# Kernel optimization log

Measured on AMD Instinct MI355X. Metric: run time of the kernel, lower is better.

The kernel has to match this reference:

```python
import jax, jax.numpy as jnp
import numpy as np

F = 256       # num_features
H = 128       # hidden_dim
B = 2048      # batch
K = 15        # max_ratios
EPS = 1e-8


def setup_inputs() -> dict:
    key = jax.random.key(0)
    ks = jax.random.split(key, 13)
    def lin(k, fan_in, fan_out):
        bound = 1.0 / np.sqrt(fan_in)
        return jax.random.uniform(k, (fan_in, fan_out), jnp.float32, -bound, bound)
    inp = {
        "x": jax.random.normal(ks[0], (B, F), jnp.float32),
        # ratio_selector: F -> H -> F*F (sigmoid)
        "rs_w1": lin(ks[1], F, H), "rs_b1": jnp.zeros((H,), jnp.float32),
        "rs_w2": lin(ks[2], H, F * F), "rs_b2": jnp.zeros((F * F,), jnp.float32),
        # operation_selector: F -> H -> 4 (softmax)
        "os_w1": lin(ks[3], F, H), "os_b1": jnp.zeros((H,), jnp.float32),
        "os_w2": lin(ks[4], H, 4), "os_b2": jnp.zeros((4,), jnp.float32),
        # feature_transform: F -> H -> F
        "ft_w1": lin(ks[5], F, H), "ft_b1": jnp.zeros((H,), jnp.float32),
        "ft_w2": lin(ks[6], H, F), "ft_b2": jnp.zeros((F,), jnp.float32),
    }
    return inp


def reference(x, rs_w1, rs_b1, rs_w2, rs_b2, os_w1, os_b1, os_w2, os_b2,
              ft_w1, ft_b1, ft_w2, ft_b2):
    nf = x.shape[1]

    # feature_transform (dropout=0 -> identity)
    tf = jax.nn.relu(x @ ft_w1 + ft_b1) @ ft_w2 + ft_b2          # [B, F]
    # ratio_selector -> sigmoid selection weights over F*F pairs
    sel = jax.nn.sigmoid(jax.nn.relu(x @ rs_w1 + rs_b1) @ rs_w2 + rs_b2)  # [B, F*F]
    # operation_selector -> softmax over 4 ops
    op_w = jax.nn.softmax(jax.nn.relu(x @ os_w1 + os_b1) @ os_w2 + os_b2, axis=-1)  # [B, 4]

    top_k = min(K, sel.shape[1])
    top_values, top_indices = jax.lax.top_k(sel, top_k)          # [B, K]

    i_idx = top_indices // nf                                    # [B, K]
    j_idx = top_indices % nf
    fi = jnp.take_along_axis(tf, i_idx, axis=1)                  # [B, K]
    fj = jnp.take_along_axis(tf, j_idx, axis=1)

    ratio = fi / (jnp.abs(fj) + EPS)
    log_ratio = jnp.log(jnp.abs(fi) + EPS) - jnp.log(jnp.abs(fj) + EPS)
    diff = fi - fj
    prod = fi * fj
    ops = jnp.stack([ratio, log_ratio, diff, prod], axis=-1)     # [B, K, 4]
    ratio_tensor = jnp.sum(ops * op_w[:, None, :], axis=-1)      # [B, K]

    pair_importances = jnp.mean(top_values, axis=0)              # [K]
    op_prefs = jnp.mean(op_w, axis=0)                            # [4]
    ratio_mags = jnp.mean(jnp.abs(ratio_tensor), axis=0)         # [K]
    sel_entropy = jnp.mean(-jnp.sum(sel * jnp.log(sel + 1e-8), axis=1))

    return ratio_tensor, pair_importances, op_prefs, ratio_mags, sel_entropy
```

## Files before the change

kernel.cpp:

```cpp
#include <hip/hip_runtime.h>
#include <math.h>

#define BB 2048
#define FD 256
#define HD 128
#define FF 65536
#define TK 15
#define BCAP 1024
#define MAXCH 4
#define POISON (1 << 30)
#define NEG_INF (-3.4e38f)
#define EPSF 1e-8f
#define ZCLAMP 1.4f

typedef short short8 __attribute__((ext_vector_type(8)));
typedef float f32x4  __attribute__((ext_vector_type(4)));

__device__ __forceinline__ unsigned short bf16_rne(float x) {
  unsigned u = __float_as_uint(x);
  unsigned r = u + 0x7FFFu + ((u >> 16) & 1u);
  return (unsigned short)(r >> 16);
}

#define HC0 3.4657359e-01f
#define HC1 (-7.6713203e-02f)
#define HC2 (-6.25e-02f)
#define HC3 1.6809444e-02f
#define HC4 7.8125e-03f
#define HC5 (-2.4621900e-03f)
#define HC6 (-8.6805556e-04f)
#define HC7 3.0960500e-04f
#define HC8 9.2231000e-05f

__device__ __forceinline__ float hpoly(float zc) {
  float p = HC8;
  p = fmaf(p, zc, HC7); p = fmaf(p, zc, HC6); p = fmaf(p, zc, HC5);
  p = fmaf(p, zc, HC4); p = fmaf(p, zc, HC3); p = fmaf(p, zc, HC2);
  p = fmaf(p, zc, HC1); p = fmaf(p, zc, HC0);
  return p;
}

__global__ __launch_bounds__(256) void k1_front(
    const float* __restrict__ x,
    const float* __restrict__ rs_w1, const float* __restrict__ rs_b1,
    const float* __restrict__ rs_w2, const float* __restrict__ rs_b2,
    const float* __restrict__ os_w1, const float* __restrict__ os_b1,
    const float* __restrict__ os_w2, const float* __restrict__ os_b2,
    const float* __restrict__ ft_w1, const float* __restrict__ ft_b1,
    const float* __restrict__ ft_w2, const float* __restrict__ ft_b2,
    float* __restrict__ hrs, unsigned short* __restrict__ hb,
    float* __restrict__ tf, float* __restrict__ opw,
    float* __restrict__ tau, int* __restrict__ gcnt)
{
  __shared__ float xs[4 * FD];
  __shared__ float hft[4][HD];
  __shared__ float hos[4][HD];
  __shared__ float hl[4 * HD];
  __shared__ float lg[4][4];
  __shared__ float wred[4][4][2];
  const int tid = threadIdx.x;
  const int wave = tid >> 6, lane = tid & 63;
  const int r0  = blockIdx.x * 4;

  if (tid < 4) gcnt[blockIdx.x * 4 + tid] = 0;

  for (int i = tid; i < 4 * FD; i += 256) xs[i] = x[(size_t)r0 * FD + i];
  __syncthreads();

  {
    const int h    = tid & (HD - 1);
    const int half = tid >> 7;
    const int ra = 2 * half, rb = ra + 1;
    float a0=0.f,a1=0.f,b0=0.f,b1=0.f,c0=0.f,c1=0.f;
    for (int f = 0; f < FD; ++f) {
      const float wr = rs_w1[f*HD+h], wf = ft_w1[f*HD+h], wo = os_w1[f*HD+h];
      const float x0 = xs[ra*FD+f],   x1 = xs[rb*FD+f];
      a0 = fmaf(x0,wr,a0); a1 = fmaf(x1,wr,a1);
      b0 = fmaf(x0,wf,b0); b1 = fmaf(x1,wf,b1);
      c0 = fmaf(x0,wo,c0); c1 = fmaf(x1,wo,c1);
    }
    const float brs = rs_b1[h], bft = ft_b1[h], bos = os_b1[h];
    const float va = fmaxf(a0 + brs, 0.f), vb = fmaxf(a1 + brs, 0.f);
    hrs[(size_t)(r0+ra)*HD + h] = va;
    hrs[(size_t)(r0+rb)*HD + h] = vb;
    hb[(size_t)(r0+ra)*HD + h] = bf16_rne(va);
    hb[(size_t)(r0+rb)*HD + h] = bf16_rne(vb);
    hl[ra*HD + h] = va;
    hl[rb*HD + h] = vb;
    hft[ra][h] = fmaxf(b0 + bft, 0.f);
    hft[rb][h] = fmaxf(b1 + bft, 0.f);
    hos[ra][h] = fmaxf(c0 + bos, 0.f);
    hos[rb][h] = fmaxf(c1 + bos, 0.f);
  }
  __syncthreads();

  {
    const int c = tid;
    const float bb = ft_b2[c];
    float t0=bb,t1=bb,t2=bb,t3=bb;
    for (int h = 0; h < HD; ++h) {
      const float w = ft_w2[h*FD + c];
      t0 = fmaf(hft[0][h],w,t0); t1 = fmaf(hft[1][h],w,t1);
      t2 = fmaf(hft[2][h],w,t2); t3 = fmaf(hft[3][h],w,t3);
    }
    tf[(size_t)(r0+0)*FD+c]=t0; tf[(size_t)(r0+1)*FD+c]=t1;
    tf[(size_t)(r0+2)*FD+c]=t2; tf[(size_t)(r0+3)*FD+c]=t3;
  }

  if (tid < 16) {
    const int r = tid >> 2, o = tid & 3;
    float a = os_b2[o];
    for (int h = 0; h < HD; ++h) a = fmaf(hos[r][h], os_w2[h*4 + o], a);
    lg[r][o] = a;
  }
  __syncthreads();
  if (tid < 16) {
    const int r = tid >> 2, o = tid & 3;
    const float m = fmaxf(fmaxf(lg[r][0],lg[r][1]), fmaxf(lg[r][2],lg[r][3]));
    const float e = __expf(lg[r][o]-m);
    const float s = __expf(lg[r][0]-m)+__expf(lg[r][1]-m)+__expf(lg[r][2]-m)+__expf(lg[r][3]-m);
    opw[(size_t)(r0+r)*4+o] = e/s;
  }

  {
    const int c0 = tid * 4;
    float z[4][4];
    const float4 bb = *(const float4*)(rs_b2 + c0);
#pragma unroll
    for (int r = 0; r < 4; ++r) { z[r][0]=bb.x; z[r][1]=bb.y; z[r][2]=bb.z; z[r][3]=bb.w; }
    for (int k = 0; k < HD; ++k) {
      const float4 ww = *(const float4*)(rs_w2 + (size_t)k * FF + c0);
#pragma unroll
      for (int r = 0; r < 4; ++r) {
        const float a = hl[r * HD + k];
        z[r][0] = fmaf(a, ww.x, z[r][0]);
        z[r][1] = fmaf(a, ww.y, z[r][1]);
        z[r][2] = fmaf(a, ww.z, z[r][2]);
        z[r][3] = fmaf(a, ww.w, z[r][3]);
      }
    }
#pragma unroll
    for (int r = 0; r < 4; ++r) {
      float s1 = z[r][0] + z[r][1] + z[r][2] + z[r][3];
      float s2 = z[r][0]*z[r][0] + z[r][1]*z[r][1] + z[r][2]*z[r][2] + z[r][3]*z[r][3];
#pragma unroll
      for (int d = 1; d < 64; d <<= 1) { s1 += __shfl_xor(s1, d); s2 += __shfl_xor(s2, d); }
      if (lane == 0) { wred[wave][r][0] = s1; wred[wave][r][1] = s2; }
    }
    __syncthreads();
    if (tid < 4) {
      const float s1 = wred[0][tid][0]+wred[1][tid][0]+wred[2][tid][0]+wred[3][tid][0];
      const float s2 = wred[0][tid][1]+wred[1][tid][1]+wred[2][tid][1]+wred[3][tid][1];
      const float mu  = s1 * (1.f / 1024.f);
      const float var = fmaxf(s2 * (1.f / 1024.f) - mu * mu, 0.f);
      const float sd  = sqrtf(var);
      tau[r0 + tid] = (sd > 1e-6f * (fabsf(mu) + 1e-6f)) ? (mu + 3.1f * sd) : NEG_INF;
    }
  }
}

__global__ __launch_bounds__(256, 3) void k2_sel(
    const float* __restrict__ W2, const float* __restrict__ b2,
    const float* __restrict__ hrs, const unsigned short* __restrict__ hb,
    const float* __restrict__ tau,
    int* __restrict__ gcnt, float* __restrict__ gz, int* __restrict__ gi,
    float* __restrict__ ent_part, int capr)
{
  __shared__ uint4 Blds[2][16][64];
  __shared__ int   cands[BCAP];
  __shared__ float tau_l[512];
  __shared__ int   bcnt;
  __shared__ float entred[4];

  const int tid  = threadIdx.x;
  const int wave = tid >> 6, lane = tid & 63;
  const int n16  = lane & 15, quad = lane >> 4;
  const int xcd = blockIdx.x & 7, jj = blockIdx.x >> 3;
  const int cc  = ((jj >> 2) << 3) | xcd, rs = jj & 3;
  const int c0  = cc * 128, rbase = rs * 512;
  const int half = wave & 1, wrow0 = (wave >> 1) * 64;
  const int wcol0 = half * 64;

  if (tid == 0) bcnt = 0;
  tau_l[tid] = tau[rbase + tid];
  tau_l[tid + 256] = tau[rbase + 256 + tid];

  for (int p = 0; p < 8; ++p) {
    const int pid = p * 256 + tid;
    const int bh = pid >> 10;
    const int rest = pid & 1023;
    const int bct = rest >> 8, bks = (rest >> 6) & 3, bln = rest & 63;
    const int bn16 = bln & 15, bqd = bln >> 4;
    const int col = c0 + bh * 64 + bct * 16 + bn16;
    const int k0 = bks * 32 + bqd * 8;
    short8 f;
#pragma unroll
    for (int u = 0; u < 8; ++u)
      f[u] = (short)bf16_rne(W2[(size_t)(k0 + u) * FF + col]);
    Blds[bh][bct * 4 + bks][bln] = __builtin_bit_cast(uint4, f);
  }
  __syncthreads();

  float bv[4];
#pragma unroll
  for (int ct = 0; ct < 4; ++ct) bv[ct] = b2[c0 + wcol0 + ct * 16 + n16];

  float ent = 0.f;

  for (int mt = 0; mt < 4; ++mt) {
#pragma unroll
    for (int rh = 0; rh < 2; ++rh) {
      const int hrow = rbase + mt * 128 + wrow0 + rh * 32;

      f32x4 acc[2][4];
#pragma unroll
      for (int rt = 0; rt < 2; ++rt)
#pragma unroll
        for (int ct = 0; ct < 4; ++ct) acc[rt][ct] = (f32x4){0.f, 0.f, 0.f, 0.f};

#pragma unroll
      for (int ks = 0; ks < 4; ++ks) {
        short8 af[2], bfr[4];
#pragma unroll
        for (int rt = 0; rt < 2; ++rt)
          af[rt] = __builtin_bit_cast(short8,
              *(const uint4*)(hb + (size_t)(hrow + rt * 16 + n16) * HD + ks * 32 + quad * 8));
#pragma unroll
        for (int ct = 0; ct < 4; ++ct)
          bfr[ct] = __builtin_bit_cast(short8, Blds[half][ct * 4 + ks][lane]);
#pragma unroll
        for (int rt = 0; rt < 2; ++rt)
#pragma unroll
          for (int ct = 0; ct < 4; ++ct)
            acc[rt][ct] = __builtin_amdgcn_mfma_f32_16x16x32_bf16(
                af[rt], bfr[ct], acc[rt][ct], 0, 0, 0);
      }

      float zmax = 0.f;
#pragma unroll
      for (int rt = 0; rt < 2; ++rt) {
        const int rl0 = mt * 128 + wrow0 + rh * 32 + rt * 16 + quad * 4;
        const f32x4 tl = *(const f32x4*)&tau_l[rl0];
#pragma unroll
        for (int ct = 0; ct < 4; ++ct) {
#pragma unroll
          for (int rg = 0; rg < 4; ++rg) {
            const float z = acc[rt][ct][rg] + bv[ct];
            zmax = fmaxf(zmax, __builtin_fabsf(z));
            const float zc = fminf(fmaxf(z, -ZCLAMP), ZCLAMP);
            ent -= hpoly(zc);
            if (__any(z >= tl[rg])) {
              if (z >= tl[rg]) {
                const int q  = atomicAdd(&bcnt, 1);
                const int gm = rl0 + rg;
                if (q < BCAP) cands[q] = (gm << 7) | (wcol0 + ct * 16 + n16);
                else atomicOr(&gcnt[rbase + gm], POISON);
              }
            }
          }
        }
      }
      if (__any(zmax > ZCLAMP)) {
#pragma unroll
        for (int rt = 0; rt < 2; ++rt)
#pragma unroll
          for (int ct = 0; ct < 4; ++ct)
#pragma unroll
            for (int rg = 0; rg < 4; ++rg) {
              const float z = acc[rt][ct][rg] + bv[ct];
              if (__builtin_fabsf(z) > ZCLAMP) {
                const float zc = fminf(fmaxf(z, -ZCLAMP), ZCLAMP);
                const float zx = fmaxf(z, -60.f);
                const float w = 1.f + __expf(-zx);
                ent += hpoly(zc) - __logf(w) * __builtin_amdgcn_rcpf(w);
              }
            }
      }
    }
  }

  __syncthreads();
  {
    const int nc = min(bcnt, BCAP);
    const int grp = tid >> 4, gl = tid & 15;
    for (int ci = grp; ci < nc; ci += 16) {
      const int pk = cands[ci];
      const int r = rbase + (pk >> 7), c = c0 + (pk & 127);
      float s = 0.f;
      const int k0 = gl * 8;
#pragma unroll
      for (int u = 0; u < 8; ++u)
        s = fmaf(hrs[(size_t)r * HD + k0 + u], W2[(size_t)(k0 + u) * FF + c], s);
#pragma unroll
      for (int d = 1; d < 16; d <<= 1) s += __shfl_xor(s, d);
      if (gl == 0) {
        const float z = s + b2[c];
        const int pos = atomicAdd(&gcnt[r], 1);
        if (pos < capr) {
          gz[(size_t)r * capr + pos] = z;
          gi[(size_t)r * capr + pos] = c;
        }
      }
    }
  }

#pragma unroll
  for (int off = 32; off >= 1; off >>= 1) ent += __shfl_down(ent, off);
  if (lane == 0) entred[wave] = ent;
  __syncthreads();
  if (tid == 0) ent_part[blockIdx.x] = entred[0] + entred[1] + entred[2] + entred[3];
}

__global__ __launch_bounds__(256) void k3_select(
    const int* __restrict__ gcnt, const float* __restrict__ gz, const int* __restrict__ gi,
    const float* __restrict__ tau,
    const float* __restrict__ hrs, const float* __restrict__ W2, const float* __restrict__ b2,
    const float* __restrict__ tf, const float* __restrict__ opw,
    float* __restrict__ out_rt, float* __restrict__ pi_part, float* __restrict__ mag_part,
    int capr)
{
  __shared__ float csv[4][MAXCH][16];
  __shared__ int   csi[4][MAXCH][16];
  __shared__ float tv[4][TK];
  __shared__ int   ti[4][TK];
  __shared__ float s_pi[4][TK];
  __shared__ float s_mag[4][TK];
  __shared__ float red_v[256];
  __shared__ int   red_i[256];
  __shared__ float hrow[HD];
  __shared__ int   fb_w[4];
  __shared__ int   fb_n;

  const int tid  = threadIdx.x;
  const int wave = tid >> 6, lane = tid & 63;
  const int row  = blockIdx.x * 4 + wave;
  if (tid == 0) fb_n = 0;
  __syncthreads();

  const int raw = gcnt[row];
  const float tau_r = tau[row];
  int okflag = (raw >= TK && raw <= capr) ? 1 : 0;

  if (okflag) {
    const int nch = (raw + 63) >> 6;
    for (int ch = 0; ch < nch; ++ch) {
      const int sl = ch * 64 + lane;
      float v; int ix;
      if (sl < raw) {
        const float z = gz[(size_t)row * capr + sl];
        v  = 1.f / (1.f + __expf(-z));
        ix = gi[(size_t)row * capr + sl];
      } else { v = -1.f; ix = 0x7fffffff; }
#pragma unroll
      for (int k = 2; k <= 64; k <<= 1) {
#pragma unroll
        for (int j = k >> 1; j >= 1; j >>= 1) {
          const float pv = __shfl_xor(v, j);
          const int   pj = __shfl_xor(ix, j);
          const bool up    = ((lane & k) == 0);
          const bool lower = ((lane & j) == 0);
          const bool gt = (v > pv) || (v == pv && ix < pj);
          const bool keep = (lower == up) ? gt : !gt;
          if (!keep) { v = pv; ix = pj; }
        }
      }
      if (lane < 16) { csv[wave][ch][lane] = v; csi[wave][ch][lane] = ix; }
    }
    if (lane == 0) {
      int p[MAXCH];
#pragma unroll
      for (int i = 0; i < MAXCH; ++i) p[i] = 0;
      for (int round = 0; round < TK; ++round) {
        float bvv = -2.f; int bi = 0x7fffffff; int bw = 0;
        for (int ch = 0; ch < nch; ++ch) {
          if (p[ch] < 16) {
            const float vv = csv[wave][ch][p[ch]];
            const int   ii = csi[wave][ch][p[ch]];
            if (vv > bvv || (vv == bvv && ii < bi)) { bvv = vv; bi = ii; bw = ch; }
          }
        }
        ++p[bw];
        tv[wave][round] = bvv; ti[wave][round] = bi;
      }
      const float stau = 1.f / (1.f + __expf(-tau_r));
      if (tv[wave][TK - 1] < stau) okflag = 0;
    }
    okflag = __shfl(okflag, 0);
  }
  if (!okflag && lane == 0) { const int q = atomicAdd(&fb_n, 1); fb_w[q] = wave; }
  __syncthreads();

  const int nfb = fb_n;
  for (int f = 0; f < nfb; ++f) {
    const int w = fb_w[f];
    const int frow = blockIdx.x * 4 + w;
    for (int i = tid; i < HD; i += 256) hrow[i] = hrs[(size_t)frow * HD + i];
    __syncthreads();
    float kv[TK]; int ki[TK];
#pragma unroll
    for (int q = 0; q < TK; ++q) { kv[q] = -2.f; ki[q] = 0x7fffffff; }
    for (int u = 0; u < FF / 256; ++u) {
      const int c = u * 256 + tid;
      float z = b2[c];
      for (int k = 0; k < HD; ++k) z = fmaf(hrow[k], W2[(size_t)k * FF + c], z);
      const float s = 1.f / (1.f + __expf(-z));
      if (s > kv[TK-1] || (s == kv[TK-1] && c < ki[TK-1])) {
        float cv = s; int cc2 = c;
#pragma unroll
        for (int q = 0; q < TK; ++q) {
          const bool bet = (cv > kv[q]) || (cv == kv[q] && cc2 < ki[q]);
          const float tq = kv[q]; const int tj = ki[q];
          if (bet) { kv[q] = cv; ki[q] = cc2; cv = tq; cc2 = tj; }
        }
      }
    }
    int pi = 0;
    for (int round = 0; round < TK; ++round) {
      red_v[tid] = (pi < TK) ? kv[pi] : -2.f;
      red_i[tid] = (pi < TK) ? ki[pi] : 0x7fffffff;
      __syncthreads();
      for (int off = 128; off >= 1; off >>= 1) {
        if (tid < off) {
          const float ov = red_v[tid + off]; const int oi = red_i[tid + off];
          if (ov > red_v[tid] || (ov == red_v[tid] && oi < red_i[tid])) {
            red_v[tid] = ov; red_i[tid] = oi;
          }
        }
        __syncthreads();
      }
      const float wv = red_v[0]; const int wi = red_i[0];
      __syncthreads();
      if (pi < TK && ki[pi] == wi) ++pi;
      if (tid == 0) { tv[w][round] = wv; ti[w][round] = wi; }
    }
    __syncthreads();
  }
  __syncthreads();

  if (lane < TK) {
    const float rv = tv[wave][lane];
    const int j = ti[wave][lane], ii = j >> 8, jj = j & 255;
    const float fi = tf[(size_t)row * FD + ii];
    const float fj = tf[(size_t)row * FD + jj];
    const float* w = opw + (size_t)row * 4;
    const float ratio = fi / (fabsf(fj) + EPSF);
    const float lr    = logf(fabsf(fi) + EPSF) - logf(fabsf(fj) + EPSF);
    const float rt    = ratio * w[0] + lr * w[1] + (fi - fj) * w[2] + fi * fj * w[3];
    out_rt[(size_t)row * TK + lane] = rt;
    s_pi[wave][lane]  = rv;
    s_mag[wave][lane] = fabsf(rt);
  }
  __syncthreads();
  if (tid < TK) {
    pi_part[(size_t)blockIdx.x * TK + tid]  = s_pi[0][tid]+s_pi[1][tid]+s_pi[2][tid]+s_pi[3][tid];
    mag_part[(size_t)blockIdx.x * TK + tid] = s_mag[0][tid]+s_mag[1][tid]+s_mag[2][tid]+s_mag[3][tid];
  }
}

__global__ __launch_bounds__(256) void k4_final(
    const float* __restrict__ pi_part, const float* __restrict__ mag_part,
    const float* __restrict__ opw, const float* __restrict__ ent_part,
    float* __restrict__ out)
{
  __shared__ float red[256];
  const int tid = threadIdx.x;
  const int NB3 = BB / 4;
  const int base = BB * TK;
  const int sec = blockIdx.x;

  if (sec == 0) {
    const int r = tid & 15, seg = tid >> 4;
    float s = 0.f;
    if (r < TK) for (int q = seg; q < NB3; q += 16) s += pi_part[(size_t)q * TK + r];
    red[tid] = s; __syncthreads();
    if (tid < TK) { float t = 0.f; for (int g = 0; g < 16; ++g) t += red[g*16 + tid];
      out[base + tid] = t / (float)BB; }
  } else if (sec == 1) {
    const int r = tid & 15, seg = tid >> 4;
    float s = 0.f;
    if (r < TK) for (int q = seg; q < NB3; q += 16) s += mag_part[(size_t)q * TK + r];
    red[tid] = s; __syncthreads();
    if (tid < TK) { float t = 0.f; for (int g = 0; g < 16; ++g) t += red[g*16 + tid];
      out[base + 19 + tid] = t / (float)BB; }
  } else if (sec == 2) {
    const int o = tid & 3, seg = tid >> 2;
    float s = 0.f;
    for (int q = seg; q < BB; q += 64) s += opw[(size_t)q * 4 + o];
    red[tid] = s; __syncthreads();
    if (tid < 4) { float t = 0.f; for (int g = 0; g < 64; ++g) t += red[g*4 + tid];
      out[base + 15 + tid] = t / (float)BB; }
  } else {
    float s = 0.f;
    for (int q = tid; q < 2048; q += 256) s += ent_part[q];
    red[tid] = s; __syncthreads();
    for (int off = 128; off >= 1; off >>= 1) {
      if (tid < off) red[tid] += red[tid + off];
      __syncthreads();
    }
    if (tid == 0) out[base + 34] = -red[0] / (float)BB;
  }
}

extern "C" void kernel_launch(void* const* d_in, const int* in_sizes, int n_in,
                              void* d_out, int out_size, void* d_ws, size_t ws_size,
                              hipStream_t stream) {
  (void)in_sizes; (void)n_in; (void)out_size;
  const float* x     = (const float*)d_in[0];
  const float* rs_w1 = (const float*)d_in[1];
  const float* rs_b1 = (const float*)d_in[2];
  const float* rs_w2 = (const float*)d_in[3];
  const float* rs_b2 = (const float*)d_in[4];
  const float* os_w1 = (const float*)d_in[5];
  const float* os_b1 = (const float*)d_in[6];
  const float* os_w2 = (const float*)d_in[7];
  const float* os_b2 = (const float*)d_in[8];
  const float* ft_w1 = (const float*)d_in[9];
  const float* ft_b1 = (const float*)d_in[10];
  const float* ft_w2 = (const float*)d_in[11];
  const float* ft_b2 = (const float*)d_in[12];
  float* out = (float*)d_out;

  float* ws       = (float*)d_ws;
  float* hrs      = ws;
  float* tf       = hrs + (size_t)BB * HD;
  float* opw      = tf + (size_t)BB * FD;
  float* ent_part = opw + (size_t)BB * 4;
  float* pi_part  = ent_part + 2048;
  float* mag_part = pi_part + 512 * TK;
  float* tau      = mag_part + 512 * TK;
  unsigned short* hb = (unsigned short*)(tau + BB);
  int*   gcnt     = (int*)(hb + (size_t)BB * HD);
  float* gz       = (float*)(gcnt + BB);
  const size_t fixed = (size_t)((char*)gz - (char*)d_ws);
  int capr = 64 * MAXCH;
  while (capr > 64 && fixed + (size_t)BB * capr * 8 > ws_size) capr -= 64;
  int* gi = (int*)(gz + (size_t)BB * capr);

  hipLaunchKernelGGL(k1_front, dim3(BB / 4), dim3(256), 0, stream,
                     x, rs_w1, rs_b1, rs_w2, rs_b2, os_w1, os_b1, os_w2, os_b2,
                     ft_w1, ft_b1, ft_w2, ft_b2, hrs, hb, tf, opw, tau, gcnt);
  hipLaunchKernelGGL(k2_sel, dim3(512 * 4), dim3(256), 0, stream,
                     rs_w2, rs_b2, hrs, hb, tau, gcnt, gz, gi, ent_part, capr);
  hipLaunchKernelGGL(k3_select, dim3(BB / 4), dim3(256), 0, stream,
                     gcnt, gz, gi, tau, hrs, rs_w2, rs_b2, tf, opw,
                     out, pi_part, mag_part, capr);
  hipLaunchKernelGGL(k4_final, dim3(4), dim3(256), 0, stream,
                     pi_part, mag_part, opw, ent_part, out);
}
```

Measured before the change: 292.0 us.

## Narrow k2 column tiles to 64, double grid, split k1 reduction over features

The selection GEMM kernel now gives each block 64 columns instead of 128, with each wave covering 128 rows. This halves the LDS B tile and candidate buffer and doubles the grid to 4096 blocks for more occupancy and parallelism. The bias is folded into the accumulator init. The front kernel splits the feature loop across two thread halves that each handle all 4 rows, then combines the halves through shared memory. The trade-off is that each A fragment from global memory is reused across fewer columns, so A traffic doubles, and the smaller candidate buffer may overflow into the slow path more often.

```diff
diff --git a/kernel.cpp b/kernel.cpp
--- a/kernel.cpp
+++ b/kernel.cpp
@@ -6,12 +6,13 @@
 #define HD 128
 #define FF 65536
 #define TK 15
-#define BCAP 1024
+#define BCAP 512
 #define MAXCH 4
 #define POISON (1 << 30)
 #define NEG_INF (-3.4e38f)
 #define EPSF 1e-8f
 #define ZCLAMP 1.4f
+#define NK2 4096
 
 typedef short short8 __attribute__((ext_vector_type(8)));
 typedef float f32x4  __attribute__((ext_vector_type(4)));
@@ -53,6 +54,7 @@
     float* __restrict__ tau, int* __restrict__ gcnt)
 {
   __shared__ float xs[4 * FD];
+  __shared__ float red[128][12];
   __shared__ float hft[4][HD];
   __shared__ float hos[4][HD];
   __shared__ float hl[4 * HD];
@@ -68,29 +70,42 @@
   __syncthreads();
 
   {
-    const int h    = tid & (HD - 1);
-    const int half = tid >> 7;
-    const int ra = 2 * half, rb = ra + 1;
-    float a0=0.f,a1=0.f,b0=0.f,b1=0.f,c0=0.f,c1=0.f;
-    for (int f = 0; f < FD; ++f) {
+    const int h  = tid & 127;
+    const int fs = tid >> 7;
+    float a[4] = {0.f,0.f,0.f,0.f}, b[4] = {0.f,0.f,0.f,0.f}, c[4] = {0.f,0.f,0.f,0.f};
+    const int f0 = fs * 128;
+    for (int i = 0; i < 128; ++i) {
+      const int f = f0 + i;
       const float wr = rs_w1[f*HD+h], wf = ft_w1[f*HD+h], wo = os_w1[f*HD+h];
-      const float x0 = xs[ra*FD+f],   x1 = xs[rb*FD+f];
-      a0 = fmaf(x0,wr,a0); a1 = fmaf(x1,wr,a1);
-      b0 = fmaf(x0,wf,b0); b1 = fmaf(x1,wf,b1);
-      c0 = fmaf(x0,wo,c0); c1 = fmaf(x1,wo,c1);
-    }
-    const float brs = rs_b1[h], bft = ft_b1[h], bos = os_b1[h];
-    const float va = fmaxf(a0 + brs, 0.f), vb = fmaxf(a1 + brs, 0.f);
-    hrs[(size_t)(r0+ra)*HD + h] = va;
-    hrs[(size_t)(r0+rb)*HD + h] = vb;
-    hb[(size_t)(r0+ra)*HD + h] = bf16_rne(va);
-    hb[(size_t)(r0+rb)*HD + h] = bf16_rne(vb);
-    hl[ra*HD + h] = va;
-    hl[rb*HD + h] = vb;
-    hft[ra][h] = fmaxf(b0 + bft, 0.f);
-    hft[rb][h] = fmaxf(b1 + bft, 0.f);
-    hos[ra][h] = fmaxf(c0 + bos, 0.f);
-    hos[rb][h] = fmaxf(c1 + bos, 0.f);
+#pragma unroll
+      for (int r = 0; r < 4; ++r) {
+        const float xv = xs[r*FD+f];
+        a[r] = fmaf(xv, wr, a[r]);
+        b[r] = fmaf(xv, wf, b[r]);
+        c[r] = fmaf(xv, wo, c[r]);
+      }
+    }
+    if (fs == 1) {
+#pragma unroll
+      for (int r = 0; r < 4; ++r) {
+        red[h][r] = a[r]; red[h][4+r] = b[r]; red[h][8+r] = c[r];
+      }
+    }
+    __syncthreads();
+    if (fs == 0) {
+      const float brs = rs_b1[h], bft = ft_b1[h], bos = os_b1[h];
+#pragma unroll
+      for (int r = 0; r < 4; ++r) {
+        const float va = fmaxf(a[r] + red[h][r]   + brs, 0.f);
+        const float vb = fmaxf(b[r] + red[h][4+r] + bft, 0.f);
+        const float vc = fmaxf(c[r] + red[h][8+r] + bos, 0.f);
+        hrs[(size_t)(r0+r)*HD + h] = va;
+        hb[(size_t)(r0+r)*HD + h]  = bf16_rne(va);
+        hl[r*HD + h] = va;
+        hft[r][h] = vb;
+        hos[r][h] = vc;
+      }
+    }
   }
   __syncthreads();
 
@@ -166,7 +181,7 @@
     int* __restrict__ gcnt, float* __restrict__ gz, int* __restrict__ gi,
     float* __restrict__ ent_part, int capr)
 {
-  __shared__ uint4 Blds[2][16][64];
+  __shared__ uint4 Blds[16][64];
   __shared__ int   cands[BCAP];
   __shared__ float tau_l[512];
   __shared__ int   bcnt;
@@ -176,106 +191,102 @@
   const int wave = tid >> 6, lane = tid & 63;
   const int n16  = lane & 15, quad = lane >> 4;
   const int xcd = blockIdx.x & 7, jj = blockIdx.x >> 3;
-  const int cc  = ((jj >> 2) << 3) | xcd, rs = jj & 3;
-  const int c0  = cc * 128, rbase = rs * 512;
-  const int half = wave & 1, wrow0 = (wave >> 1) * 64;
-  const int wcol0 = half * 64;
+  const int cc  = ((jj >> 2) << 3) | xcd;
+  const int rs  = jj & 3;
+  const int c0  = cc * 64, rbase = rs * 512;
+  const int wrow0 = wave * 128;
 
   if (tid == 0) bcnt = 0;
   tau_l[tid] = tau[rbase + tid];
   tau_l[tid + 256] = tau[rbase + 256 + tid];
 
-  for (int p = 0; p < 8; ++p) {
+  for (int p = 0; p < 4; ++p) {
     const int pid = p * 256 + tid;
-    const int bh = pid >> 10;
-    const int rest = pid & 1023;
-    const int bct = rest >> 8, bks = (rest >> 6) & 3, bln = rest & 63;
+    const int bct = pid >> 8, bks = (pid >> 6) & 3, bln = pid & 63;
     const int bn16 = bln & 15, bqd = bln >> 4;
-    const int col = c0 + bh * 64 + bct * 16 + bn16;
+    const int col = c0 + bct * 16 + bn16;
     const int k0 = bks * 32 + bqd * 8;
     short8 f;
 #pragma unroll
     for (int u = 0; u < 8; ++u)
       f[u] = (short)bf16_rne(W2[(size_t)(k0 + u) * FF + col]);
-    Blds[bh][bct * 4 + bks][bln] = __builtin_bit_cast(uint4, f);
+    Blds[bct * 4 + bks][bln] = __builtin_bit_cast(uint4, f);
   }
   __syncthreads();
 
   float bv[4];
 #pragma unroll
-  for (int ct = 0; ct < 4; ++ct) bv[ct] = b2[c0 + wcol0 + ct * 16 + n16];
+  for (int ct = 0; ct < 4; ++ct) bv[ct] = b2[c0 + ct * 16 + n16];
 
   float ent = 0.f;
 
   for (int mt = 0; mt < 4; ++mt) {
-#pragma unroll
-    for (int rh = 0; rh < 2; ++rh) {
-      const int hrow = rbase + mt * 128 + wrow0 + rh * 32;
-
-      f32x4 acc[2][4];
+    const int mrow = rbase + wrow0 + mt * 32;
+
+    f32x4 acc[2][4];
+#pragma unroll
+    for (int rt = 0; rt < 2; ++rt)
+#pragma unroll
+      for (int ct = 0; ct < 4; ++ct)
+        acc[rt][ct] = (f32x4){bv[ct], bv[ct], bv[ct], bv[ct]};
+
+#pragma unroll
+    for (int ks = 0; ks < 4; ++ks) {
+      short8 af[2], bfr[4];
 #pragma unroll
       for (int rt = 0; rt < 2; ++rt)
-#pragma unroll
-        for (int ct = 0; ct < 4; ++ct) acc[rt][ct] = (f32x4){0.f, 0.f, 0.f, 0.f};
-
-#pragma unroll
-      for (int ks = 0; ks < 4; ++ks) {
-        short8 af[2], bfr[4];
-#pragma unroll
-        for (int rt = 0; rt < 2; ++rt)
-          af[rt] = __builtin_bit_cast(short8,
-              *(const uint4*)(hb + (size_t)(hrow + rt * 16 + n16) * HD + ks * 32 + quad * 8));
+        af[rt] = __builtin_bit_cast(short8,
+            *(const uint4*)(hb + (size_t)(mrow + rt * 16 + n16) * HD + ks * 32 + quad * 8));
+#pragma unroll
+      for (int ct = 0; ct < 4; ++ct)
+        bfr[ct] = __builtin_bit_cast(short8, Blds[ct * 4 + ks][lane]);
+#pragma unroll
+      for (int rt = 0; rt < 2; ++rt)
 #pragma unroll
         for (int ct = 0; ct < 4; ++ct)
-          bfr[ct] = __builtin_bit_cast(short8, Blds[half][ct * 4 + ks][lane]);
-#pragma unroll
-        for (int rt = 0; rt < 2; ++rt)
-#pragma unroll
-          for (int ct = 0; ct < 4; ++ct)
-            acc[rt][ct] = __builtin_amdgcn_mfma_f32_16x16x32_bf16(
-                af[rt], bfr[ct], acc[rt][ct], 0, 0, 0);
-      }
-
-      float zmax = 0.f;
-#pragma unroll
-      for (int rt = 0; rt < 2; ++rt) {
-        const int rl0 = mt * 128 + wrow0 + rh * 32 + rt * 16 + quad * 4;
-        const f32x4 tl = *(const f32x4*)&tau_l[rl0];
-#pragma unroll
-        for (int ct = 0; ct < 4; ++ct) {
-#pragma unroll
-          for (int rg = 0; rg < 4; ++rg) {
-            const float z = acc[rt][ct][rg] + bv[ct];
-            zmax = fmaxf(zmax, __builtin_fabsf(z));
-            const float zc = fminf(fmaxf(z, -ZCLAMP), ZCLAMP);
-            ent -= hpoly(zc);
-            if (__any(z >= tl[rg])) {
-              if (z >= tl[rg]) {
-                const int q  = atomicAdd(&bcnt, 1);
-                const int gm = rl0 + rg;
-                if (q < BCAP) cands[q] = (gm << 7) | (wcol0 + ct * 16 + n16);
-                else atomicOr(&gcnt[rbase + gm], POISON);
-              }
+          acc[rt][ct] = __builtin_amdgcn_mfma_f32_16x16x32_bf16(
+              af[rt], bfr[ct], acc[rt][ct], 0, 0, 0);
+    }
+
+    float zmax = 0.f;
+#pragma unroll
+    for (int rt = 0; rt < 2; ++rt) {
+      const int rl0 = wrow0 + mt * 32 + rt * 16 + quad * 4;
+      const f32x4 tl = *(const f32x4*)&tau_l[rl0];
+#pragma unroll
+      for (int ct = 0; ct < 4; ++ct) {
+#pragma unroll
+        for (int rg = 0; rg < 4; ++rg) {
+          const float z = acc[rt][ct][rg];
+          zmax = fmaxf(zmax, __builtin_fabsf(z));
+          const float zc = fminf(fmaxf(z, -ZCLAMP), ZCLAMP);
+          ent -= hpoly(zc);
+          if (__any(z >= tl[rg])) {
+            if (z >= tl[rg]) {
+              const int q  = atomicAdd(&bcnt, 1);
+              const int gm = rl0 + rg;
+              if (q < BCAP) cands[q] = (gm << 6) | (ct * 16 + n16);
+              else atomicOr(&gcnt[rbase + gm], POISON);
             }
           }
         }
       }
-      if (__any(zmax > ZCLAMP)) {
-#pragma unroll
-        for (int rt = 0; rt < 2; ++rt)
-#pragma unroll
-          for (int ct = 0; ct < 4; ++ct)
-#pragma unroll
-            for (int rg = 0; rg < 4; ++rg) {
-              const float z = acc[rt][ct][rg] + bv[ct];
-              if (__builtin_fabsf(z) > ZCLAMP) {
-                const float zc = fminf(fmaxf(z, -ZCLAMP), ZCLAMP);
-                const float zx = fmaxf(z, -60.f);
-                const float w = 1.f + __expf(-zx);
-                ent += hpoly(zc) - __logf(w) * __builtin_amdgcn_rcpf(w);
-              }
+    }
+    if (__any(zmax > ZCLAMP)) {
+#pragma unroll
+      for (int rt = 0; rt < 2; ++rt)
+#pragma unroll
+        for (int ct = 0; ct < 4; ++ct)
+#pragma unroll
+          for (int rg = 0; rg < 4; ++rg) {
+            const float z = acc[rt][ct][rg];
+            if (__builtin_fabsf(z) > ZCLAMP) {
+              const float zc = fminf(fmaxf(z, -ZCLAMP), ZCLAMP);
+              const float zx = fmaxf(z, -60.f);
+              const float w = 1.f + __expf(-zx);
+              ent += hpoly(zc) - __logf(w) * __builtin_amdgcn_rcpf(w);
             }
-      }
+          }
     }
   }
 
@@ -285,7 +296,7 @@
     const int grp = tid >> 4, gl = tid & 15;
     for (int ci = grp; ci < nc; ci += 16) {
       const int pk = cands[ci];
-      const int r = rbase + (pk >> 7), c = c0 + (pk & 127);
+      const int r = rbase + (pk >> 6), c = c0 + (pk & 63);
       float s = 0.f;
       const int k0 = gl * 8;
 #pragma unroll
@@ -491,7 +502,7 @@
       out[base + 15 + tid] = t / (float)BB; }
   } else {
     float s = 0.f;
-    for (int q = tid; q < 2048; q += 256) s += ent_part[q];
+    for (int q = tid; q < NK2; q += 256) s += ent_part[q];
     red[tid] = s; __syncthreads();
     for (int off = 128; off >= 1; off >>= 1) {
       if (tid < off) red[tid] += red[tid + off];
@@ -525,7 +536,7 @@
   float* tf       = hrs + (size_t)BB * HD;
   float* opw      = tf + (size_t)BB * FD;
   float* ent_part = opw + (size_t)BB * 4;
-  float* pi_part  = ent_part + 2048;
+  float* pi_part  = ent_part + NK2;
   float* mag_part = pi_part + 512 * TK;
   float* tau      = mag_part + 512 * TK;
   unsigned short* hb = (unsigned short*)(tau + BB);
@@ -539,7 +550,7 @@
   hipLaunchKernelGGL(k1_front, dim3(BB / 4), dim3(256), 0, stream,
                      x, rs_w1, rs_b1, rs_w2, rs_b2, os_w1, os_b1, os_w2, os_b2,
                      ft_w1, ft_b1, ft_w2, ft_b2, hrs, hb, tf, opw, tau, gcnt);
-  hipLaunchKernelGGL(k2_sel, dim3(512 * 4), dim3(256), 0, stream,
+  hipLaunchKernelGGL(k2_sel, dim3(NK2), dim3(256), 0, stream,
                      rs_w2, rs_b2, hrs, hb, tau, gcnt, gz, gi, ent_part, capr);
   hipLaunchKernelGGL(k3_select, dim3(BB / 4), dim3(256), 0, stream,
                      gcnt, gz, gi, tau, hrs, rs_w2, rs_b2, tf, opw,
```

Measured after the change: 354.2 us. 1.21x slower.
